# Optimization experiments

Measured on AMD Instinct MI355X. Metric: run time of the kernel, lower is better.

Reference implementation:

```python
import jax, jax.numpy as jnp
import numpy as np

I, O, H, M, N = 64, 64, 512, 64, 128  # input, output, controller hidden, content bits, addresses
B, S = 32, 256
EPS = 1e-8
R_SZ = M + 6          # read head: key(M) + beta(1) + gate(1) + shift(3) + gamma(1)
W_SZ = 3 * M + 6      # write head: read params + erase(M) + add(M)


def _split_head(p, with_erase_add):
    k = jnp.tanh(p[:, :M])
    beta = jax.nn.softplus(p[:, M:M + 1])
    g = jax.nn.sigmoid(p[:, M + 1:M + 2])
    s = jax.nn.softmax(p[:, M + 2:M + 5], axis=-1)
    gamma = 1.0 + jax.nn.softplus(p[:, M + 5:M + 6])
    if with_erase_add:
        e = jax.nn.sigmoid(p[:, M + 6:2 * M + 6])
        a = jnp.tanh(p[:, 2 * M + 6:3 * M + 6])
        return k, beta, g, s, gamma, e, a
    return k, beta, g, s, gamma


def _address(k, beta, g, s, gamma, w_prev, mem):
    # k:[B,M] beta,g,gamma:[B,1] s:[B,3] w_prev:[B,N] mem:[B,N,M]
    knorm = jnp.linalg.norm(k, axis=-1, keepdims=True)   # [B,1]
    mnorm = jnp.linalg.norm(mem, axis=-1)                # [B,N]
    sim = jnp.einsum('bm,bnm->bn', k, mem) / (knorm * mnorm + EPS)
    wc = jax.nn.softmax(beta * sim, axis=-1)             # content addressing
    wg = g * wc + (1.0 - g) * w_prev                     # interpolation gate
    # circular convolution with shifts {-1, 0, +1}
    rolled = jnp.stack([jnp.roll(wg, o, axis=-1) for o in (-1, 0, 1)], axis=-1)  # [B,N,3]
    ws = jnp.einsum('bnt,bt->bn', rolled, s)
    wp = jnp.power(jnp.maximum(ws, 1e-12), gamma)        # sharpening
    return wp / jnp.sum(wp, axis=-1, keepdims=True)


def setup_inputs() -> dict:
    key = jax.random.key(0)
    ks = jax.random.split(key, 5)
    sc = 0.05
    ctrl_in = I + M + H  # external input + read vector + recurrent hidden
    return {
        'inputs': jax.random.normal(ks[0], (B, S, I), jnp.float32),
        'W_lstm': jax.random.normal(ks[1], (ctrl_in, 4 * H), jnp.float32) * sc,
        'b_lstm': jnp.zeros((4 * H,), jnp.float32),
        'W_int': jax.random.normal(ks[2], (H, R_SZ + W_SZ), jnp.float32) * sc,
        'b_int': jnp.zeros((R_SZ + W_SZ,), jnp.float32),
        'W_out': jax.random.normal(ks[3], (H + M, O), jnp.float32) * sc,
        'b_out': jnp.zeros((O,), jnp.float32),
    }


def reference(inputs, W_lstm, b_lstm, W_int, b_int, W_out, b_out):
    Bsz = inputs.shape[0]
    mem0 = jnp.full((Bsz, N, M), 0.01, jnp.float32)
    w0 = jnp.zeros((Bsz, N), jnp.float32).at[:, 0].set(1.0)
    h0 = jnp.zeros((Bsz, H), jnp.float32)
    c0 = jnp.zeros((Bsz, H), jnp.float32)
    r0 = jnp.full((Bsz, M), 0.01, jnp.float32)

    def step(carry, x_t):
        h, c, w_r, w_w, mem, r = carry
        # LSTM controller over [input, read vector]
        z = jnp.concatenate([x_t, r, h], axis=-1) @ W_lstm + b_lstm
        i_g, f_g, g_g, o_g = jnp.split(z, 4, axis=-1)
        c = jax.nn.sigmoid(f_g) * c + jax.nn.sigmoid(i_g) * jnp.tanh(g_g)
        h = jax.nn.sigmoid(o_g) * jnp.tanh(c)
        # interface parameters
        p = h @ W_int + b_int
        rk, rb, rg, rs, rgam = _split_head(p[:, :R_SZ], False)
        wk, wb, wg_, ws_, wgam, e, a = _split_head(p[:, R_SZ:], True)
        # write (erase then add), then read from updated memory
        w_w = _address(wk, wb, wg_, ws_, wgam, w_w, mem)
        mem = mem * (1.0 - w_w[:, :, None] * e[:, None, :]) + w_w[:, :, None] * a[:, None, :]
        w_r = _address(rk, rb, rg, rs, rgam, w_r, mem)
        r = jnp.einsum('bn,bnm->bm', w_r, mem)
        out = jnp.concatenate([h, r], axis=-1) @ W_out + b_out
        return (h, c, w_r, w_w, mem, r), out

    xs = jnp.swapaxes(inputs, 0, 1)  # [S,B,I]
    _, outs = jax.lax.scan(step, (h0, c0, w0, w0, mem0, r0), xs)
    return jnp.swapaxes(outs, 0, 1)  # [B,S,O]
```

## Files before the change

kernel.cpp:

```cpp
#include <hip/hip_runtime.h>
#include <hip/hip_fp16.h>
#include <math.h>

#define NI 64
#define NO 64
#define NH 512
#define NM 64
#define NN 128
#define NB 32
#define NS 256
#define ZD 2048
#define PD 268
#define NG 128
#define GBLK 160
#define TPB 512
#define UPB 4
#define ST 580
#define RS_ST 68
#define PP_ST 272

__device__ __forceinline__ float sigm(float x){ return 1.0f/(1.0f+expf(-x)); }
__device__ __forceinline__ float softplus_(float x){ return (x>15.f)? x : log1pf(expf(x)); }

__device__ __forceinline__ float cloadf(const float* p){
  return __hip_atomic_load(p, __ATOMIC_RELAXED, __HIP_MEMORY_SCOPE_SYSTEM);
}
__device__ __forceinline__ void cstoref(float* p, float v){
  __hip_atomic_store(p, v, __ATOMIC_RELAXED, __HIP_MEMORY_SCOPE_SYSTEM);
}
__device__ __forceinline__ float2 cloadf2(const float* p){
  unsigned long long u = __hip_atomic_load((const unsigned long long*)p,
                                           __ATOMIC_RELAXED, __HIP_MEMORY_SCOPE_SYSTEM);
  return __builtin_bit_cast(float2, u);
}
__device__ __forceinline__ unsigned long long cload8(const void* p){
  return __hip_atomic_load((const unsigned long long*)p,
                           __ATOMIC_RELAXED, __HIP_MEMORY_SCOPE_SYSTEM);
}
__device__ __forceinline__ void cstore8(void* p, unsigned long long v){
  __hip_atomic_store((unsigned long long*)p, v,
                     __ATOMIC_RELAXED, __HIP_MEMORY_SCOPE_SYSTEM);
}
__device__ __forceinline__ int cloadi(const int* p){
  return __hip_atomic_load(p, __ATOMIC_RELAXED, __HIP_MEMORY_SCOPE_SYSTEM);
}
__device__ __forceinline__ void cstorei(int* p, int v){
  __hip_atomic_store(p, v, __ATOMIC_RELAXED, __HIP_MEMORY_SCOPE_SYSTEM);
}
__device__ __forceinline__ void caddi(int* p){
  __hip_atomic_fetch_add(p, 1, __ATOMIC_RELAXED, __HIP_MEMORY_SCOPE_SYSTEM);
}

__device__ __forceinline__ unsigned long long packh4(float a, float b, float c, float d){
  unsigned short u0 = __builtin_bit_cast(unsigned short, __float2half(a));
  unsigned short u1 = __builtin_bit_cast(unsigned short, __float2half(b));
  unsigned short u2 = __builtin_bit_cast(unsigned short, __float2half(c));
  unsigned short u3 = __builtin_bit_cast(unsigned short, __float2half(d));
  return (unsigned long long)u0 | ((unsigned long long)u1 << 16)
       | ((unsigned long long)u2 << 32) | ((unsigned long long)u3 << 48);
}
__device__ __forceinline__ void unpackh4(unsigned long long v, float* o){
  o[0] = __half2float(__builtin_bit_cast(__half, (unsigned short)(v      )));
  o[1] = __half2float(__builtin_bit_cast(__half, (unsigned short)(v >> 16)));
  o[2] = __half2float(__builtin_bit_cast(__half, (unsigned short)(v >> 32)));
  o[3] = __half2float(__builtin_bit_cast(__half, (unsigned short)(v >> 48)));
}

__device__ __forceinline__ void postFlag(int* flags, int idx, int era){
  __syncthreads();
  if (threadIdx.x == 0) cstorei(&flags[idx*16], era);
}
__device__ __forceinline__ void waitAll32(const int* flags, int era){
  if (threadIdx.x < 32) {
    while (cloadi(&flags[(int)threadIdx.x*16]) < era)
      __builtin_amdgcn_s_sleep(1);
  }
  __syncthreads();
}
__device__ __forceinline__ void postCnt(int* c){
  __syncthreads();
  if (threadIdx.x == 0) caddi(c);
}
__device__ __forceinline__ void waitCnt(const int* c, int target){
  if (threadIdx.x == 0) {
    while (cloadi(c) < target) __builtin_amdgcn_s_sleep(2);
  }
  __syncthreads();
}

struct P1S { float inT[NB*ST]; float zpart[4*16*32]; float rs[NB*RS_ST]; float hx[4*33]; };
struct P2S { float h[132]; float pp[544]; };
struct P3S { float h[NH]; float p[PD+4];
             float rk[NM], wk[NM], e[NM], a[NM];
             float sim[NN]; float red[8*64]; float r[NM]; };
union  USH { P1S p1; P2S p2; P3S p3; };

__device__ void address_head(int t, const float* __restrict__ ks,
                             const float* __restrict__ scal,
                             float* __restrict__ w_arr,
                             const float* __restrict__ mem_s,
                             float* __restrict__ sim_s)
{
  {
    int n = t >> 2, sub = t & 3;
    int cn = (n & 7) << 2;
    float dot = 0.f, sq = 0.f;
#pragma unroll
    for (int i = 0; i < 16; i += 4) {
      int m = sub*16 + i;
      float4 mv = *(const float4*)&mem_s[n*NM + (m ^ cn)];
      float4 kv = *(const float4*)&ks[m];
      dot = fmaf(kv.x, mv.x, dot); dot = fmaf(kv.y, mv.y, dot);
      dot = fmaf(kv.z, mv.z, dot); dot = fmaf(kv.w, mv.w, dot);
      sq  = fmaf(mv.x, mv.x, sq);  sq  = fmaf(mv.y, mv.y, sq);
      sq  = fmaf(mv.z, mv.z, sq);  sq  = fmaf(mv.w, mv.w, sq);
    }
    dot += __shfl_xor(dot, 1); sq += __shfl_xor(sq, 1);
    dot += __shfl_xor(dot, 2); sq += __shfl_xor(sq, 2);
    if (sub == 0) sim_s[n] = dot / (scal[0]*sqrtf(sq) + 1e-8f);
  }
  __syncthreads();
  if (t < 64) {
    int l = t;
    float beta = scal[1], g = scal[2], s0 = scal[3], s1 = scal[4], s2 = scal[5], gamma = scal[6];
    float x0 = beta*sim_s[l], x1 = beta*sim_s[l+64];
    float mx = fmaxf(x0, x1);
#pragma unroll
    for (int off=32; off; off>>=1) mx = fmaxf(mx, __shfl_xor(mx, off));
    float e0 = expf(x0-mx), e1 = expf(x1-mx);
    float sm = e0+e1;
#pragma unroll
    for (int off=32; off; off>>=1) sm += __shfl_xor(sm, off);
    float inv = 1.0f/sm;
    float wg0 = g*e0*inv + (1.f-g)*w_arr[l];
    float wg1 = g*e1*inv + (1.f-g)*w_arr[l+64];
    float up0 = __shfl(wg0, (l+1)&63);
    float w1f = __shfl(wg1, 0);
    float plus0 = (l==63) ? w1f : up0;
    float dn0 = __shfl(wg0, (l-1)&63);
    float w1b = __shfl(wg1, 63);
    float minus0 = (l==0) ? w1b : dn0;
    float up1 = __shfl(wg1, (l+1)&63);
    float w0f = __shfl(wg0, 0);
    float plus1 = (l==63) ? w0f : up1;
    float dn1 = __shfl(wg1, (l-1)&63);
    float w0b = __shfl(wg0, 63);
    float minus1 = (l==0) ? w0b : dn1;
    float ws0 = s0*plus0 + s1*wg0 + s2*minus0;
    float ws1 = s0*plus1 + s1*wg1 + s2*minus1;
    float wp0 = powf(fmaxf(ws0, 1e-12f), gamma);
    float wp1 = powf(fmaxf(ws1, 1e-12f), gamma);
    float tot = wp0+wp1;
#pragma unroll
    for (int off=32; off; off>>=1) tot += __shfl_xor(tot, off);
    float invt = 1.0f/tot;
    w_arr[l]    = wp0*invt;
    w_arr[l+64] = wp1*invt;
  }
  __syncthreads();
}

extern "C" __global__ __launch_bounds__(TPB, 1)
void ntm_coop(const float* __restrict__ inputs, const float* __restrict__ W_lstm,
              const float* __restrict__ b_lstm, const float* __restrict__ W_int,
              const float* __restrict__ b_int, const float* __restrict__ W_out,
              const float* __restrict__ b_out, float* __restrict__ out,
              float* __restrict__ wsf)
{
  __shared__ float mem_s[NN*NM];
  __shared__ float wr_s[NN], ww_s[NN];
  __shared__ float scal_s[14];
  __shared__ USH u;

  int*    cbase   = (int*)wsf;
  int*    flags_r = (int*)wsf + 1024;
  __half* hT16    = (__half*)(wsf + 8192);
  float*  rT    = wsf + 8192 + 16384;
  float*  pPart = rT + NB*NM;
  float*  WrT   = pPart + 2*NB*4*PP_ST;
  float*  WintT = WrT + ZD*64;
  float*  WoutT = WintT + PD*NH;

  const int t   = threadIdx.x;
  const int bid = blockIdx.x;
  const bool isB = (bid < NB);

  {
    int gid = bid*TPB + t;
    for (int idx = gid; idx < PD*NH; idx += GBLK*TPB) {
      int c = idx >> 9, k = idx & 511;
      cstoref(&WintT[idx], W_int[(size_t)k*PD + c]);
    }
    for (int idx = gid; idx < NO*576; idx += GBLK*TPB) {
      int c = idx / 576, k = idx - c*576;
      cstoref(&WoutT[idx], W_out[(size_t)k*NO + c]);
    }
    for (int idx = gid; idx < ZD*64; idx += GBLK*TPB) {
      int c = idx >> 6, k = idx & 63;
      cstoref(&WrT[idx], W_lstm[(size_t)(64 + k)*ZD + c]);
    }
  }
  postCnt(&cbase[256]);
  waitCnt(&cbase[256], GBLK);

  if (!isB) {
    const int gb   = bid - NB;
    const int pb_  = t & 31;
    const int gate = (t >> 5) & 3;
    const int kp   = t >> 7;
    const int j0   = ((gb & 7) << 6) + ((gb >> 3) * UPB);
    const int colg = gate*NH + j0;
    const int pj   = t >> 5;
    const int pw   = t & 31;
    const int q_g  = gb & 7;
    const int bp   = gb & 31;
    const int hp   = gb >> 5;
    float c_reg = 0.f;
    __syncthreads();

    for (int step = 0; step < NS; ++step) {
      const __half* h16_prev = hT16 + (size_t)((step & 1) ^ 1)*NH*NB;
      __half*       h16_cur  = hT16 + (size_t)(step & 1)*NH*NB;

      if (step) {
        if (t < 8) {
          const int tgt = 16*step;
          while (cloadi(&cbase[t*16]) < tgt) __builtin_amdgcn_s_sleep(1);
        }
        __syncthreads();
      }

      { int sb = t >> 4, k4 = (t & 15) * 4;
        float4 xv = *(const float4*)(inputs + ((size_t)sb*NS + step)*NI + k4);
        *(float4*)&u.p1.inT[sb*ST + k4] = xv; }
      if (step == 0) {
#pragma unroll
        for (int i = 0; i < 8; ++i) {
          int q = t + 512*i; int b_ = q >> 7, u_ = (q & 127) * 4;
          *(float4*)&u.p1.inT[b_*ST + 64 + u_] = make_float4(0.f,0.f,0.f,0.f);
        }
      } else {
#pragma unroll
        for (int i = 0; i < 8; ++i) {
          int q = t + 512*i; int b_ = q >> 7, u_ = (q & 127) * 4;
          unsigned long long v = cload8(h16_prev + b_*NH + u_);
          float o[4]; unpackh4(v, o);
          *(float4*)&u.p1.inT[b_*ST + 64 + u_] = make_float4(o[0],o[1],o[2],o[3]);
        }
      }
      __syncthreads();

      float a0=0.f, a1=0.f, a2=0.f, a3=0.f;
      {
        const float* xr = &u.p1.inT[pb_*ST + kp*16];
        const float* Wp = W_lstm + (size_t)(kp*16)*ZD + colg;
#pragma unroll
        for (int k4 = 0; k4 < 16; k4 += 4) {
          float4 x = *(const float4*)&xr[k4];
          float4 w0 = *(const float4*)(Wp + (size_t)(k4+0)*ZD);
          float4 w1 = *(const float4*)(Wp + (size_t)(k4+1)*ZD);
          float4 w2 = *(const float4*)(Wp + (size_t)(k4+2)*ZD);
          float4 w3 = *(const float4*)(Wp + (size_t)(k4+3)*ZD);
          a0 = fmaf(x.x, w0.x, a0); a1 = fmaf(x.x, w0.y, a1);
          a2 = fmaf(x.x, w0.z, a2); a3 = fmaf(x.x, w0.w, a3);
          a0 = fmaf(x.y, w1.x, a0); a1 = fmaf(x.y, w1.y, a1);
          a2 = fmaf(x.y, w1.z, a2); a3 = fmaf(x.y, w1.w, a3);
          a0 = fmaf(x.z, w2.x, a0); a1 = fmaf(x.z, w2.y, a1);
          a2 = fmaf(x.z, w2.z, a2); a3 = fmaf(x.z, w2.w, a3);
          a0 = fmaf(x.w, w3.x, a0); a1 = fmaf(x.w, w3.y, a1);
          a2 = fmaf(x.w, w3.z, a2); a3 = fmaf(x.w, w3.w, a3);
        }
        const float* hr = &u.p1.inT[pb_*ST + 64 + kp*128];
        const float* Wh = W_lstm + (size_t)(128 + kp*128)*ZD + colg;
#pragma unroll 4
        for (int k4 = 0; k4 < 128; k4 += 4) {
          float4 x = *(const float4*)&hr[k4];
          float4 w0 = *(const float4*)(Wh + (size_t)(k4+0)*ZD);
          float4 w1 = *(const float4*)(Wh + (size_t)(k4+1)*ZD);
          float4 w2 = *(const float4*)(Wh + (size_t)(k4+2)*ZD);
          float4 w3 = *(const float4*)(Wh + (size_t)(k4+3)*ZD);
          a0 = fmaf(x.x, w0.x, a0); a1 = fmaf(x.x, w0.y, a1);
          a2 = fmaf(x.x, w0.z, a2); a3 = fmaf(x.x, w0.w, a3);
          a0 = fmaf(x.y, w1.x, a0); a1 = fmaf(x.y, w1.y, a1);
          a2 = fmaf(x.y, w1.z, a2); a3 = fmaf(x.y, w1.w, a3);
          a0 = fmaf(x.z, w2.x, a0); a1 = fmaf(x.z, w2.y, a1);
          a2 = fmaf(x.z, w2.z, a2); a3 = fmaf(x.z, w2.w, a3);
          a0 = fmaf(x.w, w3.x, a0); a1 = fmaf(x.w, w3.y, a1);
          a2 = fmaf(x.w, w3.z, a2); a3 = fmaf(x.w, w3.w, a3);
        }
        if (step == 0) {
          const float* Wr0 = W_lstm + (size_t)(64 + kp*16)*ZD + colg;
#pragma unroll
          for (int k = 0; k < 16; ++k) {
            float4 w = *(const float4*)(Wr0 + (size_t)k*ZD);
            a0 = fmaf(0.01f, w.x, a0); a1 = fmaf(0.01f, w.y, a1);
            a2 = fmaf(0.01f, w.z, a2); a3 = fmaf(0.01f, w.w, a3);
          }
        }
      }
      { int base = (kp*16 + gate*4)*32 + pb_;
        u.p1.zpart[base]    = a0;
        u.p1.zpart[base+32] = a1;
        u.p1.zpart[base+64] = a2;
        u.p1.zpart[base+96] = a3; }

      if (step) {
        waitAll32(flags_r, step);
        { int e = 2*t; int bb = e >> 6, kk = e & 63;
          float2 v = cloadf2(rT + e);
          *(float2*)&u.p1.rs[bb*RS_ST + kk] = v;
          e += 1024; bb = e >> 6; kk = e & 63;
          v = cloadf2(rT + e);
          *(float2*)&u.p1.rs[bb*RS_ST + kk] = v; }
      }
      __syncthreads();

      if (t < 128) {
        float zrv[4] = {0.f, 0.f, 0.f, 0.f};
        if (step) {
          const float* rr = &u.p1.rs[pw*RS_ST];
#pragma unroll
          for (int gt = 0; gt < 4; ++gt) {
            const float* Wc = WrT + (size_t)(gt*NH + j0 + pj)*64;
            float acc = 0.f;
#pragma unroll
            for (int k = 0; k < 64; k += 4) {
              float4 w = *(const float4*)&Wc[k];
              acc = fmaf(rr[k],   w.x, acc);
              acc = fmaf(rr[k+1], w.y, acc);
              acc = fmaf(rr[k+2], w.z, acc);
              acc = fmaf(rr[k+3], w.w, acc);
            }
            zrv[gt] = acc;
          }
        }
        float zv[4];
#pragma unroll
        for (int gt = 0; gt < 4; ++gt) {
          int ci = gt*4 + pj;
          zv[gt] = u.p1.zpart[ci*32 + pw] + u.p1.zpart[(16+ci)*32 + pw]
                 + u.p1.zpart[(32+ci)*32 + pw] + u.p1.zpart[(48+ci)*32 + pw]
                 + zrv[gt] + b_lstm[gt*NH + j0 + pj];
        }
        float cn = sigm(zv[1])*c_reg + sigm(zv[0])*tanhf(zv[2]);
        c_reg = cn;
        u.p1.hx[pj*33 + pw] = sigm(zv[3])*tanhf(cn);
      }
      __syncthreads();
      if (t < 32) {
        unsigned long long v = packh4(u.p1.hx[t], u.p1.hx[33+t],
                                      u.p1.hx[66+t], u.p1.hx[99+t]);
        cstore8(h16_cur + t*NH + j0, v);
      }
      postCnt(&cbase[q_g*16]);

      {
        if (t < 2) {
          const int tgt = 16*(step+1);
          while (cloadi(&cbase[(2*hp + t)*16]) < tgt) __builtin_amdgcn_s_sleep(1);
        }
        __syncthreads();
      }
      if (t < 32) {
        unsigned long long v = cload8(h16_cur + bp*NH + hp*128 + 4*t);
        float o[4]; unpackh4(v, o);
        u.p2.h[4*t]   = o[0];
        u.p2.h[4*t+1] = o[1];
        u.p2.h[4*t+2] = o[2];
        u.p2.h[4*t+3] = o[3];
      }
      __syncthreads();
      {
        int c = t >> 1, kh = t & 1;
        const float* Wc = WintT + (size_t)c*512 + hp*128 + kh*64;
        const float* hh = &u.p2.h[kh*64];
        float acc = 0.f;
#pragma unroll
        for (int k = 0; k < 64; k += 4) {
          float4 w = *(const float4*)&Wc[k];
          acc = fmaf(hh[k],   w.x, acc);
          acc = fmaf(hh[k+1], w.y, acc);
          acc = fmaf(hh[k+2], w.z, acc);
          acc = fmaf(hh[k+3], w.w, acc);
        }
        u.p2.pp[t] = acc;
        if (t < 24) {
          int id = 512 + t; int c2 = id >> 1; int k2 = id & 1;
          const float* Wc2 = WintT + (size_t)c2*512 + hp*128 + k2*64;
          const float* hh2 = &u.p2.h[k2*64];
          float ac2 = 0.f;
#pragma unroll
          for (int k = 0; k < 64; k += 4) {
            float4 w = *(const float4*)&Wc2[k];
            ac2 = fmaf(hh2[k],   w.x, ac2);
            ac2 = fmaf(hh2[k+1], w.y, ac2);
            ac2 = fmaf(hh2[k+2], w.z, ac2);
            ac2 = fmaf(hh2[k+3], w.w, ac2);
          }
          u.p2.pp[id] = ac2;
        }
      }
      __syncthreads();
      if (t < PD) {
        float sv = u.p2.pp[2*t] + u.p2.pp[2*t+1];
        cstoref(&pPart[(((size_t)(step&1)*NB + bp)*4 + hp)*PP_ST + t], sv);
      }
      postCnt(&cbase[512 + bp*16]);
    }
  } else {
    const int b = bid;
    for (int i = t; i < NN*NM; i += TPB) mem_s[i] = 0.01f;
    if (t < NN) { wr_s[t] = (t==0)?1.f:0.f; ww_s[t] = (t==0)?1.f:0.f; }
    __syncthreads();

    for (int step = 0; step < NS; ++step) {
      const int era = step + 1;
      const __half* h16_cur = hT16 + (size_t)(step & 1)*NH*NB;

      waitCnt(&cbase[512 + b*16], 4*era);
      if (t < PD) {
        float pv = b_int[t];
        const float* pb4 = &pPart[(((size_t)(step&1)*NB + b)*4)*PP_ST + t];
#pragma unroll
        for (int hp = 0; hp < 4; ++hp) pv += cloadf(pb4 + hp*PP_ST);
        u.p3.p[t] = pv;
      }
      if (t < 128) {
        unsigned long long v = cload8(h16_cur + b*NH + 4*t);
        float o[4]; unpackh4(v, o);
        *(float4*)&u.p3.h[4*t] = make_float4(o[0],o[1],o[2],o[3]);
      }
      __syncthreads();

      if (t < NM) {
        float rk = tanhf(u.p3.p[t]);
        float wk = tanhf(u.p3.p[70+t]);
        u.p3.rk[t] = rk; u.p3.wk[t] = wk;
        u.p3.e[t] = sigm(u.p3.p[140+t]);
        u.p3.a[t] = tanhf(u.p3.p[204+t]);
        float sr = rk*rk, sw = wk*wk;
#pragma unroll
        for (int off=32; off; off>>=1){ sr += __shfl_xor(sr,off); sw += __shfl_xor(sw,off); }
        if (t == 0) { scal_s[0] = sqrtf(sr); scal_s[7] = sqrtf(sw); }
      }
      if (t == 64) {
        scal_s[1] = softplus_(u.p3.p[64]);
        scal_s[2] = sigm(u.p3.p[65]);
        float a0=u.p3.p[66], a1=u.p3.p[67], a2=u.p3.p[68];
        float m = fmaxf(a0,fmaxf(a1,a2));
        float e0=expf(a0-m), e1=expf(a1-m), e2=expf(a2-m);
        float s = e0+e1+e2;
        scal_s[3]=e0/s; scal_s[4]=e1/s; scal_s[5]=e2/s;
        scal_s[6] = 1.f + softplus_(u.p3.p[69]);
      }
      if (t == 128) {
        scal_s[8]  = softplus_(u.p3.p[134]);
        scal_s[9]  = sigm(u.p3.p[135]);
        float a0=u.p3.p[136], a1=u.p3.p[137], a2=u.p3.p[138];
        float m = fmaxf(a0,fmaxf(a1,a2));
        float e0=expf(a0-m), e1=expf(a1-m), e2=expf(a2-m);
        float s = e0+e1+e2;
        scal_s[10]=e0/s; scal_s[11]=e1/s; scal_s[12]=e2/s;
        scal_s[13] = 1.f + softplus_(u.p3.p[139]);
      }
      __syncthreads();

      address_head(t, u.p3.wk, &scal_s[7], ww_s, mem_s, u.p3.sim);

      {
        int n = t >> 2, sub = t & 3;
        int cn = (n & 7) << 2;
        float w = ww_s[n];
#pragma unroll
        for (int i = 0; i < 16; i += 4) {
          int m = sub*16 + i;
          float* mp = &mem_s[n*NM + (m ^ cn)];
          float4 mv = *(float4*)mp;
          float4 ev = *(const float4*)&u.p3.e[m];
          float4 av = *(const float4*)&u.p3.a[m];
          mv.x = mv.x*(1.f - w*ev.x) + w*av.x;
          mv.y = mv.y*(1.f - w*ev.y) + w*av.y;
          mv.z = mv.z*(1.f - w*ev.z) + w*av.z;
          mv.w = mv.w*(1.f - w*ev.w) + w*av.w;
          *(float4*)mp = mv;
        }
      }
      __syncthreads();

      address_head(t, u.p3.rk, &scal_s[0], wr_s, mem_s, u.p3.sim);

      {
        int part = t >> 6, m = t & 63;
        float racc = 0.f;
#pragma unroll
        for (int nn = 0; nn < 16; ++nn) {
          int n = part*16 + nn;
          racc = fmaf(wr_s[n], mem_s[n*NM + (m ^ ((n&7)<<2))], racc);
        }
        u.p3.red[part*64 + m] = racc;
      }
      __syncthreads();
      if (t < NM) {
        float rv = 0.f;
#pragma unroll
        for (int pq = 0; pq < 8; ++pq) rv += u.p3.red[pq*64 + t];
        u.p3.r[t] = rv;
        cstoref(&rT[b*NM + t], rv);
      }
      postFlag(flags_r, b, era);

      {
        int part = t >> 6, c = t & 63;
        const float* Wc = WoutT + c*576 + part*72;
        float oacc = 0.f;
        int k0 = part*72;
#pragma unroll
        for (int kk = 0; kk < 72; kk += 4) {
          float4 w = *(const float4*)&Wc[kk];
          int k = k0 + kk;
          float v0 = (k   < NH) ? u.p3.h[k]   : u.p3.r[k-NH];
          float v1 = (k+1 < NH) ? u.p3.h[k+1] : u.p3.r[k+1-NH];
          float v2 = (k+2 < NH) ? u.p3.h[k+2] : u.p3.r[k+2-NH];
          float v3 = (k+3 < NH) ? u.p3.h[k+3] : u.p3.r[k+3-NH];
          oacc = fmaf(v0, w.x, oacc);
          oacc = fmaf(v1, w.y, oacc);
          oacc = fmaf(v2, w.z, oacc);
          oacc = fmaf(v3, w.w, oacc);
        }
        u.p3.red[part*64 + c] = oacc;
      }
      __syncthreads();
      if (t < NO) {
        float ov = b_out[t];
#pragma unroll
        for (int pq = 0; pq < 8; ++pq) ov += u.p3.red[pq*64 + t];
        out[(size_t)b*NS*NO + (size_t)step*NO + t] = ov;
      }
      __syncthreads();
    }
  }
}

extern "C" void kernel_launch(void* const* d_in, const int* in_sizes, int n_in,
                              void* d_out, int out_size, void* d_ws, size_t ws_size,
                              hipStream_t stream) {
  const float* inputs = (const float*)d_in[0];
  const float* W_lstm = (const float*)d_in[1];
  const float* b_lstm = (const float*)d_in[2];
  const float* W_int  = (const float*)d_in[3];
  const float* b_int  = (const float*)d_in[4];
  const float* W_out  = (const float*)d_in[5];
  const float* b_out  = (const float*)d_in[6];
  float* outp = (float*)d_out;
  float* wsp  = (float*)d_ws;

  hipMemsetAsync(d_ws, 0, 32768, stream);

  void* args[] = { (void*)&inputs, (void*)&W_lstm, (void*)&b_lstm,
                   (void*)&W_int, (void*)&b_int, (void*)&W_out, (void*)&b_out,
                   (void*)&outp, (void*)&wsp };
  hipLaunchCooperativeKernel((const void*)ntm_coop, dim3(GBLK), dim3(TPB),
                             args, 0, stream);
}
```

Baseline: 6.494 ms.

## Move interface projection into batch blocks and store W_int/W_out as fp16

The interface projection h@W_int no longer runs split across four gate blocks with partial sums exchanged through global memory. Each batch block now computes the full projection itself after waiting on the h-ready counters. This removes one cross-block handoff (partial-sum stores, a counter post and a wait) per step from the critical path. To cut the bandwidth of the now longer per-block dot products, W_int and W_out are stored transposed in fp16, which adds more serial work per batch block and reduces weight precision.

```diff
diff --git a/kernel.cpp b/kernel.cpp
--- a/kernel.cpp
+++ b/kernel.cpp
@@ -17,7 +17,6 @@
 #define UPB 4
 #define ST 580
 #define RS_ST 68
-#define PP_ST 272
 
 __device__ __forceinline__ float sigm(float x){ return 1.0f/(1.0f+expf(-x)); }
 __device__ __forceinline__ float softplus_(float x){ return (x>15.f)? x : log1pf(expf(x)); }
@@ -49,6 +48,9 @@
 }
 __device__ __forceinline__ void caddi(int* p){
   __hip_atomic_fetch_add(p, 1, __ATOMIC_RELAXED, __HIP_MEMORY_SCOPE_SYSTEM);
+}
+__device__ __forceinline__ void cstoreh(unsigned short* p, unsigned short v){
+  __hip_atomic_store(p, v, __ATOMIC_RELAXED, __HIP_MEMORY_SCOPE_SYSTEM);
 }
 
 __device__ __forceinline__ unsigned long long packh4(float a, float b, float c, float d){
@@ -89,11 +91,10 @@
 }
 
 struct P1S { float inT[NB*ST]; float zpart[4*16*32]; float rs[NB*RS_ST]; float hx[4*33]; };
-struct P2S { float h[132]; float pp[544]; };
-struct P3S { float h[NH]; float p[PD+4];
+struct P3S { float h[NH]; float pp[544]; float p[PD+4];
              float rk[NM], wk[NM], e[NM], a[NM];
              float sim[NN]; float red[8*64]; float r[NM]; };
-union  USH { P1S p1; P2S p2; P3S p3; };
+union  USH { P1S p1; P3S p3; };
 
 __device__ void address_head(int t, const float* __restrict__ ks,
                              const float* __restrict__ scal,
@@ -175,11 +176,10 @@
   int*    cbase   = (int*)wsf;
   int*    flags_r = (int*)wsf + 1024;
   __half* hT16    = (__half*)(wsf + 8192);
-  float*  rT    = wsf + 8192 + 16384;
-  float*  pPart = rT + NB*NM;
-  float*  WrT   = pPart + 2*NB*4*PP_ST;
-  float*  WintT = WrT + ZD*64;
-  float*  WoutT = WintT + PD*NH;
+  float*  rT      = wsf + 8192 + 16384;
+  float*  WrT     = rT + NB*NM;
+  unsigned short* WintT16 = (unsigned short*)(WrT + ZD*64);
+  unsigned short* WoutT16 = WintT16 + PD*NH;
 
   const int t   = threadIdx.x;
   const int bid = blockIdx.x;
@@ -189,11 +189,13 @@
     int gid = bid*TPB + t;
     for (int idx = gid; idx < PD*NH; idx += GBLK*TPB) {
       int c = idx >> 9, k = idx & 511;
-      cstoref(&WintT[idx], W_int[(size_t)k*PD + c]);
+      cstoreh(&WintT16[idx],
+              __builtin_bit_cast(unsigned short, __float2half(W_int[(size_t)k*PD + c])));
     }
     for (int idx = gid; idx < NO*576; idx += GBLK*TPB) {
       int c = idx / 576, k = idx - c*576;
-      cstoref(&WoutT[idx], W_out[(size_t)k*NO + c]);
+      cstoreh(&WoutT16[idx],
+              __builtin_bit_cast(unsigned short, __float2half(W_out[(size_t)k*NO + c])));
     }
     for (int idx = gid; idx < ZD*64; idx += GBLK*TPB) {
       int c = idx >> 6, k = idx & 63;
@@ -213,8 +215,6 @@
     const int pj   = t >> 5;
     const int pw   = t & 31;
     const int q_g  = gb & 7;
-    const int bp   = gb & 31;
-    const int hp   = gb >> 5;
     float c_reg = 0.f;
     __syncthreads();
 
@@ -353,59 +353,6 @@
         cstore8(h16_cur + t*NH + j0, v);
       }
       postCnt(&cbase[q_g*16]);
-
-      {
-        if (t < 2) {
-          const int tgt = 16*(step+1);
-          while (cloadi(&cbase[(2*hp + t)*16]) < tgt) __builtin_amdgcn_s_sleep(1);
-        }
-        __syncthreads();
-      }
-      if (t < 32) {
-        unsigned long long v = cload8(h16_cur + bp*NH + hp*128 + 4*t);
-        float o[4]; unpackh4(v, o);
-        u.p2.h[4*t]   = o[0];
-        u.p2.h[4*t+1] = o[1];
-        u.p2.h[4*t+2] = o[2];
-        u.p2.h[4*t+3] = o[3];
-      }
-      __syncthreads();
-      {
-        int c = t >> 1, kh = t & 1;
-        const float* Wc = WintT + (size_t)c*512 + hp*128 + kh*64;
-        const float* hh = &u.p2.h[kh*64];
-        float acc = 0.f;
-#pragma unroll
-        for (int k = 0; k < 64; k += 4) {
-          float4 w = *(const float4*)&Wc[k];
-          acc = fmaf(hh[k],   w.x, acc);
-          acc = fmaf(hh[k+1], w.y, acc);
-          acc = fmaf(hh[k+2], w.z, acc);
-          acc = fmaf(hh[k+3], w.w, acc);
-        }
-        u.p2.pp[t] = acc;
-        if (t < 24) {
-          int id = 512 + t; int c2 = id >> 1; int k2 = id & 1;
-          const float* Wc2 = WintT + (size_t)c2*512 + hp*128 + k2*64;
-          const float* hh2 = &u.p2.h[k2*64];
-          float ac2 = 0.f;
-#pragma unroll
-          for (int k = 0; k < 64; k += 4) {
-            float4 w = *(const float4*)&Wc2[k];
-            ac2 = fmaf(hh2[k],   w.x, ac2);
-            ac2 = fmaf(hh2[k+1], w.y, ac2);
-            ac2 = fmaf(hh2[k+2], w.z, ac2);
-            ac2 = fmaf(hh2[k+3], w.w, ac2);
-          }
-          u.p2.pp[id] = ac2;
-        }
-      }
-      __syncthreads();
-      if (t < PD) {
-        float sv = u.p2.pp[2*t] + u.p2.pp[2*t+1];
-        cstoref(&pPart[(((size_t)(step&1)*NB + bp)*4 + hp)*PP_ST + t], sv);
-      }
-      postCnt(&cbase[512 + bp*16]);
     }
   } else {
     const int b = bid;
@@ -417,19 +364,53 @@
       const int era = step + 1;
       const __half* h16_cur = hT16 + (size_t)(step & 1)*NH*NB;
 
-      waitCnt(&cbase[512 + b*16], 4*era);
-      if (t < PD) {
-        float pv = b_int[t];
-        const float* pb4 = &pPart[(((size_t)(step&1)*NB + b)*4)*PP_ST + t];
-#pragma unroll
-        for (int hp = 0; hp < 4; ++hp) pv += cloadf(pb4 + hp*PP_ST);
-        u.p3.p[t] = pv;
-      }
+      if (t < 8) {
+        const int tgt = 16*era;
+        while (cloadi(&cbase[t*16]) < tgt) __builtin_amdgcn_s_sleep(1);
+      }
+      __syncthreads();
+
       if (t < 128) {
         unsigned long long v = cload8(h16_cur + b*NH + 4*t);
         float o[4]; unpackh4(v, o);
         *(float4*)&u.p3.h[4*t] = make_float4(o[0],o[1],o[2],o[3]);
       }
+      __syncthreads();
+
+      {
+        int c = t >> 1, kh = t & 1;
+        const unsigned long long* Wc =
+            (const unsigned long long*)(WintT16 + (size_t)c*512 + kh*256);
+        const float* hh = u.p3.h + kh*256;
+        float pacc = 0.f;
+#pragma unroll 8
+        for (int k = 0; k < 256; k += 4) {
+          float o[4]; unpackh4(Wc[k >> 2], o);
+          pacc = fmaf(hh[k],   o[0], pacc);
+          pacc = fmaf(hh[k+1], o[1], pacc);
+          pacc = fmaf(hh[k+2], o[2], pacc);
+          pacc = fmaf(hh[k+3], o[3], pacc);
+        }
+        u.p3.pp[t] = pacc;
+        if (t < 24) {
+          int id = 512 + t; int c2 = id >> 1; int k2 = id & 1;
+          const unsigned long long* Wc2 =
+              (const unsigned long long*)(WintT16 + (size_t)c2*512 + k2*256);
+          const float* hh2 = u.p3.h + k2*256;
+          float pa2 = 0.f;
+#pragma unroll 8
+          for (int k = 0; k < 256; k += 4) {
+            float o[4]; unpackh4(Wc2[k >> 2], o);
+            pa2 = fmaf(hh2[k],   o[0], pa2);
+            pa2 = fmaf(hh2[k+1], o[1], pa2);
+            pa2 = fmaf(hh2[k+2], o[2], pa2);
+            pa2 = fmaf(hh2[k+3], o[3], pa2);
+          }
+          u.p3.pp[id] = pa2;
+        }
+      }
+      __syncthreads();
+      if (t < PD) u.p3.p[t] = u.p3.pp[2*t] + u.p3.pp[2*t+1] + b_int[t];
       __syncthreads();
 
       if (t < NM) {
@@ -511,21 +492,22 @@
 
       {
         int part = t >> 6, c = t & 63;
-        const float* Wc = WoutT + c*576 + part*72;
+        const unsigned long long* Wc =
+            (const unsigned long long*)(WoutT16 + (size_t)c*576 + part*72);
         float oacc = 0.f;
         int k0 = part*72;
 #pragma unroll
         for (int kk = 0; kk < 72; kk += 4) {
-          float4 w = *(const float4*)&Wc[kk];
+          float o[4]; unpackh4(Wc[kk >> 2], o);
           int k = k0 + kk;
           float v0 = (k   < NH) ? u.p3.h[k]   : u.p3.r[k-NH];
           float v1 = (k+1 < NH) ? u.p3.h[k+1] : u.p3.r[k+1-NH];
           float v2 = (k+2 < NH) ? u.p3.h[k+2] : u.p3.r[k+2-NH];
           float v3 = (k+3 < NH) ? u.p3.h[k+3] : u.p3.r[k+3-NH];
-          oacc = fmaf(v0, w.x, oacc);
-          oacc = fmaf(v1, w.y, oacc);
-          oacc = fmaf(v2, w.z, oacc);
-          oacc = fmaf(v3, w.w, oacc);
+          oacc = fmaf(v0, o[0], oacc);
+          oacc = fmaf(v1, o[1], oacc);
+          oacc = fmaf(v2, o[2], oacc);
+          oacc = fmaf(v3, o[3], oacc);
         }
         u.p3.red[part*64 + c] = oacc;
       }
```

Result: faster. 5.862 ms (-9.7%).
